# Performance work log

Measured on AMD Instinct MI355X. Metric: run time of the kernel, lower is better.

Reference implementation:

```python
import jax, jax.numpy as jnp
import numpy as np
import math

EMBED_DIM = 1024
NUM_HEADS = 16
HEAD_DIM = EMBED_DIM // NUM_HEADS
WINDOW_SIZE = 32  # one-sided; full window = 2*w+1 = 65
SCALING = math.sqrt(HEAD_DIM)


def setup_inputs() -> dict:
    key = jax.random.key(0)
    ks = jax.random.split(key, 9)
    B, S, E = 2, 2048, EMBED_DIM
    s = 1.0 / math.sqrt(E)
    inp = {
        "hidden_states": jax.random.normal(ks[0], (B, S, E), dtype=jnp.float32),
        "q_w": jax.random.uniform(ks[1], (E, E), jnp.float32, -s, s),
        "q_b": jax.random.uniform(ks[2], (E,), jnp.float32, -s, s),
        "k_w": jax.random.uniform(ks[3], (E, E), jnp.float32, -s, s),
        "k_b": jax.random.uniform(ks[4], (E,), jnp.float32, -s, s),
        "v_w": jax.random.uniform(ks[5], (E, E), jnp.float32, -s, s),
        "v_b": jax.random.uniform(ks[6], (E,), jnp.float32, -s, s),
        "o_w": jax.random.uniform(ks[7], (E, E), jnp.float32, -s, s),
        "o_b": jax.random.uniform(ks[8], (E,), jnp.float32, -s, s),
    }
    return inp


def reference(hidden_states, q_w, q_b, k_w, k_b, v_w, v_b, o_w, o_b):
    B, S, E = hidden_states.shape
    H, D, w = NUM_HEADS, HEAD_DIM, WINDOW_SIZE
    W = 2 * w + 1

    q = hidden_states @ q_w.T + q_b
    k = hidden_states @ k_w.T + k_b
    v = hidden_states @ v_w.T + v_b

    # [B, H, S, D]
    q = q.reshape(B, S, H, D).transpose(0, 2, 1, 3)
    k = k.reshape(B, S, H, D).transpose(0, 2, 1, 3)
    v = v.reshape(B, S, H, D).transpose(0, 2, 1, 3)

    # zero-pad seq dim by w on each side (matches F.pad value=0); padded keys
    # contribute score 0 (NOT -inf) exactly like the original unfold scheme.
    k_pad = jnp.pad(k, ((0, 0), (0, 0), (w, w), (0, 0)))
    v_pad = jnp.pad(v, ((0, 0), (0, 0), (w, w), (0, 0)))

    # window gather indices: query i sees padded positions i..i+2w (orig i-w..i+w)
    idx = jnp.arange(S)[:, None] + jnp.arange(W)[None, :]  # [S, W]
    k_slice = k_pad[:, :, idx]  # [B, H, S, W, D]
    v_slice = v_pad[:, :, idx]  # [B, H, S, W, D]

    score = jnp.einsum('bhsd,bhswd->bhsw', q, k_slice) / SCALING
    p = jax.nn.softmax(score, axis=-1)
    attn = jnp.einsum('bhsw,bhswd->bhsd', p, v_slice)

    attn = attn.transpose(0, 2, 1, 3).reshape(B, S, E)
    return attn @ o_w.T + o_b
```

## Files before the change

kernel.cpp:

```cpp
#include <hip/hip_runtime.h>
#include <math.h>

typedef _Float16 h16;
typedef _Float16 h8 __attribute__((ext_vector_type(8)));
typedef float f32x4 __attribute__((ext_vector_type(4)));

__device__ inline void gl2lds16(const void* g, void* l) {
  __builtin_amdgcn_global_load_lds(
      (const __attribute__((address_space(1))) void*)g,
      (__attribute__((address_space(3))) void*)l, 16, 0, 0);
}

__device__ inline void barrier_raw() {
  asm volatile("" ::: "memory");
  __builtin_amdgcn_s_barrier();
  asm volatile("" ::: "memory");
}

#define VMCNT(N) asm volatile("s_waitcnt vmcnt(" #N ")" ::: "memory")

__global__ __launch_bounds__(256) void f2h_all(
    const float* __restrict__ hs, const float* __restrict__ w0,
    const float* __restrict__ w1, const float* __restrict__ w2,
    const float* __restrict__ w3, h16* __restrict__ dst, int hsN) {
  int i = (blockIdx.x * 256 + threadIdx.x) * 8;
  const int tot = hsN + 4 * 1048576;
  if (i >= tot) return;
  const float* src;
  int off;
  if (i < hsN) {
    src = hs; off = i;
  } else {
    int k = i - hsN;
    int seg = k >> 20;
    off = k & 1048575;
    src = seg == 0 ? w0 : seg == 1 ? w1 : seg == 2 ? w2 : w3;
  }
  float4 a = *(const float4*)(src + off);
  float4 b = *(const float4*)(src + off + 4);
  h8 o;
  o[0] = (h16)a.x; o[1] = (h16)a.y; o[2] = (h16)a.z; o[3] = (h16)a.w;
  o[4] = (h16)b.x; o[5] = (h16)b.y; o[6] = (h16)b.z; o[7] = (h16)b.w;
  *(h8*)(dst + i) = o;
}

__global__ __launch_bounds__(256, 4) void qkv9(
    const h16* __restrict__ A, const h16* __restrict__ Bw,
    const float* __restrict__ qb, const float* __restrict__ kb,
    const float* __restrict__ vb, h16* __restrict__ qo, h16* __restrict__ ko,
    h16* __restrict__ vo) {
  __shared__ __align__(16) char smem[128 * 136 * 2];
  h16* Abuf = (h16*)smem;
  h16* Bbuf = Abuf + 2 * 128 * 32;
  h16* Csh = (h16*)smem;

  const int tid = threadIdx.x;
  const int wid = tid >> 6, lane = tid & 63;
  const int lr = lane & 15, lg = lane >> 4;
  const int wr = wid >> 1, wc = wid & 1;
  const int srow = tid >> 2;
  const int csw = ((tid & 3) ^ ((srow >> 1) & 3)) * 8;

  const int wg = (blockIdx.x & 7) * 96 + (blockIdx.x >> 3);
  const int bm = wg & 31, bn = wg >> 5;
  const int row0 = bm * 128, col0 = bn * 128;

  const h16* Ag = A + (size_t)row0 * 1024;
  const h16* Bg = Bw + (size_t)col0 * 1024;

  auto stage = [&](int t, int bi) {
    const int kof = t * 32 + csw;
    h16* Ad = Abuf + bi * 128 * 32;
    h16* Bd = Bbuf + bi * 128 * 32;
    gl2lds16(Ag + (size_t)srow * 1024 + kof, Ad + (wid * 16) * 32);
    gl2lds16(Ag + (size_t)(64 + srow) * 1024 + kof, Ad + (64 + wid * 16) * 32);
    gl2lds16(Bg + (size_t)srow * 1024 + kof, Bd + (wid * 16) * 32);
    gl2lds16(Bg + (size_t)(64 + srow) * 1024 + kof, Bd + (64 + wid * 16) * 32);
  };
  auto ldf = [&](const h16* base, int row) -> h8 {
    return *(const h8*)(base + row * 32 + (lg ^ ((row >> 1) & 3)) * 8);
  };

  f32x4 acc[4][4] = {};

  stage(0, 0);
  for (int t = 0; t < 32; ++t) {
    if (t < 31) {
      stage(t + 1, (t + 1) & 1);
      VMCNT(4);
    } else {
      VMCNT(0);
    }
    barrier_raw();
    const h16* Ar = Abuf + (t & 1) * 128 * 32;
    const h16* Br = Bbuf + (t & 1) * 128 * 32;
    h8 af[4], bf[4];
#pragma unroll
    for (int m = 0; m < 4; ++m) af[m] = ldf(Ar, wr * 64 + m * 16 + lr);
#pragma unroll
    for (int n = 0; n < 4; ++n) bf[n] = ldf(Br, wc * 64 + n * 16 + lr);
    __builtin_amdgcn_s_setprio(1);
#pragma unroll
    for (int m = 0; m < 4; ++m)
#pragma unroll
      for (int n = 0; n < 4; ++n)
        acc[m][n] =
            __builtin_amdgcn_mfma_f32_16x16x32_f16(af[m], bf[n], acc[m][n], 0, 0, 0);
    __builtin_amdgcn_s_setprio(0);
    barrier_raw();
  }

  const int tsel = bn >> 3;
  const int colseg = (bn & 7) * 128;
  const float* bp = tsel == 0 ? qb : (tsel == 1 ? kb : vb);
  h16* outp = tsel == 0 ? qo : (tsel == 1 ? ko : vo);

#pragma unroll
  for (int n = 0; n < 4; ++n) {
    const int ccol = wc * 64 + n * 16 + lr;
    const float bv = bp[colseg + ccol];
#pragma unroll
    for (int m = 0; m < 4; ++m)
#pragma unroll
      for (int j = 0; j < 4; ++j)
        Csh[(wr * 64 + m * 16 + lg * 4 + j) * 136 + ccol] =
            (h16)(acc[m][n][j] + bv);
  }
  barrier_raw();
#pragma unroll
  for (int p = 0; p < 8; ++p) {
    const int idx = p * 256 + tid;
    const int r = idx >> 4, c = idx & 15;
    h8 v = *(const h8*)&Csh[r * 136 + c * 8];
    *(h8*)&outp[(size_t)(row0 + r) * 1024 + colseg + c * 8] = v;
  }
}

__global__ __launch_bounds__(256) void oproj9(const h16* __restrict__ A,
                                              const h16* __restrict__ Bw,
                                              const float* __restrict__ b0,
                                              float* __restrict__ Cf) {
  __shared__ __align__(16) h16 Abuf[2][64][32];
  __shared__ __align__(16) h16 Bbuf[2][128][32];

  const int tid = threadIdx.x;
  const int wid = tid >> 6, lane = tid & 63;
  const int lr = lane & 15, lg = lane >> 4;
  const int wr = wid >> 1, wc = wid & 1;
  const int srow = tid >> 2;
  const int csw = ((tid & 3) ^ ((srow >> 1) & 3)) * 8;

  const int wg = (blockIdx.x & 7) * 64 + (blockIdx.x >> 3);
  const int bm = wg & 63, bn = wg >> 6;
  const int row0 = bm * 64, col0 = bn * 128;

  const h16* Ag = A + (size_t)row0 * 1024;
  const h16* Bg = Bw + (size_t)col0 * 1024;

  auto stage = [&](int t, int bi) {
    const int kof = t * 32 + csw;
    gl2lds16(Ag + (size_t)srow * 1024 + kof, &Abuf[bi][wid * 16][0]);
    gl2lds16(Bg + (size_t)srow * 1024 + kof, &Bbuf[bi][wid * 16][0]);
    gl2lds16(Bg + (size_t)(64 + srow) * 1024 + kof, &Bbuf[bi][64 + wid * 16][0]);
  };
  auto ldf = [&](const h16* base, int row) -> h8 {
    return *(const h8*)(base + row * 32 + (lg ^ ((row >> 1) & 3)) * 8);
  };

  f32x4 acc[2][4] = {};

  stage(0, 0);
  for (int t = 0; t < 32; ++t) {
    if (t < 31) {
      stage(t + 1, (t + 1) & 1);
      VMCNT(3);
    } else {
      VMCNT(0);
    }
    barrier_raw();
    const h16* Ar = &Abuf[t & 1][0][0];
    const h16* Br = &Bbuf[t & 1][0][0];
    h8 af[2], bf[4];
#pragma unroll
    for (int m = 0; m < 2; ++m) af[m] = ldf(Ar, wr * 32 + m * 16 + lr);
#pragma unroll
    for (int n = 0; n < 4; ++n) bf[n] = ldf(Br, wc * 64 + n * 16 + lr);
    __builtin_amdgcn_s_setprio(1);
#pragma unroll
    for (int m = 0; m < 2; ++m)
#pragma unroll
      for (int n = 0; n < 4; ++n)
        acc[m][n] =
            __builtin_amdgcn_mfma_f32_16x16x32_f16(af[m], bf[n], acc[m][n], 0, 0, 0);
    __builtin_amdgcn_s_setprio(0);
    barrier_raw();
  }

#pragma unroll
  for (int n = 0; n < 4; ++n) {
    const int cidx = col0 + wc * 64 + n * 16 + lr;
    const float bv = b0[cidx];
#pragma unroll
    for (int m = 0; m < 2; ++m)
#pragma unroll
      for (int j = 0; j < 4; ++j) {
        const int r = row0 + wr * 32 + m * 16 + lg * 4 + j;
        Cf[(size_t)r * 1024 + cidx] = acc[m][n][j] + bv;
      }
  }
}

__global__ __launch_bounds__(256) void swattn(const h16* __restrict__ Q,
                                              const h16* __restrict__ K,
                                              const h16* __restrict__ V,
                                              h16* __restrict__ O) {
  __shared__ __align__(16) h16 Ksh[128 * 72];
  __shared__ __align__(16) h16 Vsh[64 * 136];
  __shared__ __align__(16) h16 Psh[4][16 * 136];

  const int qb0 = blockIdx.x * 64;
  const int bh = blockIdx.y;
  const int b = bh >> 4, h = bh & 15;
  const int tid = threadIdx.x;
  const int wave = tid >> 6, lane = tid & 63;
  const int lr = lane & 15, lg = lane >> 4;

  const h16* Qb = Q + (size_t)b * 2048 * 1024 + h * 64;
  const h16* Kb = K + (size_t)b * 2048 * 1024 + h * 64;
  const h16* Vb = V + (size_t)b * 2048 * 1024 + h * 64;

#pragma unroll
  for (int i = 0; i < 4; ++i) {
    const int c = tid * 4 + i;
    const int row = c >> 3, c8 = c & 7;
    const int t = qb0 - 32 + row;
    h8 kv, vv;
    if (t >= 0 && t < 2048) {
      kv = *(const h8*)&Kb[(size_t)t * 1024 + c8 * 8];
      vv = *(const h8*)&Vb[(size_t)t * 1024 + c8 * 8];
    } else {
#pragma unroll
      for (int j = 0; j < 8; ++j) { kv[j] = (h16)0.f; vv[j] = (h16)0.f; }
    }
    *(h8*)&Ksh[row * 72 + c8 * 8] = kv;
#pragma unroll
    for (int j = 0; j < 8; ++j) Vsh[(c8 * 8 + j) * 136 + row] = vv[j];
  }
  __syncthreads();

  const int qrow = qb0 + wave * 16 + lr;
  h8 qa[2];
#pragma unroll
  for (int kk = 0; kk < 2; ++kk)
    qa[kk] = *(const h8*)&Qb[(size_t)qrow * 1024 + kk * 32 + lg * 8];

  f32x4 sacc[8] = {};
#pragma unroll
  for (int n = 0; n < 8; ++n)
#pragma unroll
    for (int kk = 0; kk < 2; ++kk) {
      h8 kb = *(const h8*)&Ksh[(n * 16 + lr) * 72 + kk * 32 + lg * 8];
      sacc[n] = __builtin_amdgcn_mfma_f32_16x16x32_f16(qa[kk], kb, sacc[n], 0, 0, 0);
    }

  float p[8][4];
#pragma unroll
  for (int j = 0; j < 4; ++j) {
    const int wrow = wave * 16 + lg * 4 + j;
    float mx = -1e30f;
#pragma unroll
    for (int n = 0; n < 8; ++n) {
      const int d = n * 16 + lr - wrow;
      float s = (d < 0 || d > 64) ? -1e30f : sacc[n][j] * 0.125f;
      p[n][j] = s;
      mx = fmaxf(mx, s);
    }
#pragma unroll
    for (int off = 1; off < 16; off <<= 1) mx = fmaxf(mx, __shfl_xor(mx, off, 64));
    float sum = 0.f;
#pragma unroll
    for (int n = 0; n < 8; ++n) {
      const float e = __expf(p[n][j] - mx);
      p[n][j] = e;
      sum += e;
    }
#pragma unroll
    for (int off = 1; off < 16; off <<= 1) sum += __shfl_xor(sum, off, 64);
    const float inv = 1.f / sum;
#pragma unroll
    for (int n = 0; n < 8; ++n) p[n][j] *= inv;
  }

#pragma unroll
  for (int n = 0; n < 8; ++n)
#pragma unroll
    for (int j = 0; j < 4; ++j)
      Psh[wave][(lg * 4 + j) * 136 + n * 16 + lr] = (h16)p[n][j];
  __syncthreads();

  f32x4 oacc[4] = {};
#pragma unroll
  for (int kk = 0; kk < 4; ++kk) {
    h8 pa = *(const h8*)&Psh[wave][lr * 136 + kk * 32 + lg * 8];
#pragma unroll
    for (int n = 0; n < 4; ++n) {
      h8 vb = *(const h8*)&Vsh[(n * 16 + lr) * 136 + kk * 32 + lg * 8];
      oacc[n] = __builtin_amdgcn_mfma_f32_16x16x32_f16(pa, vb, oacc[n], 0, 0, 0);
    }
  }

#pragma unroll
  for (int n = 0; n < 4; ++n)
#pragma unroll
    for (int j = 0; j < 4; ++j) {
      const int s = qb0 + wave * 16 + lg * 4 + j;
      const int d = n * 16 + lr;
      O[((size_t)b * 2048 + s) * 1024 + h * 64 + d] = (h16)oacc[n][j];
    }
}

extern "C" void kernel_launch(void* const* d_in, const int* in_sizes, int n_in,
                              void* d_out, int out_size, void* d_ws, size_t ws_size,
                              hipStream_t stream) {
  const float* hs = (const float*)d_in[0];
  const float* qw = (const float*)d_in[1];
  const float* qb = (const float*)d_in[2];
  const float* kw = (const float*)d_in[3];
  const float* kb = (const float*)d_in[4];
  const float* vw = (const float*)d_in[5];
  const float* vb = (const float*)d_in[6];
  const float* ow = (const float*)d_in[7];
  const float* ob = (const float*)d_in[8];

  const int M = in_sizes[0] / 1024;

  h16* hsH = (h16*)d_ws;
  h16* wqkv = hsH + (size_t)M * 1024;
  h16* woH = wqkv + (size_t)3072 * 1024;
  h16* qH = woH + (size_t)1024 * 1024;
  h16* kH = qH + (size_t)M * 1024;
  h16* vH = kH + (size_t)M * 1024;
  h16* attnH = vH + (size_t)M * 1024;

  const int tot = M * 1024 + 4 * 1048576;
  f2h_all<<<(tot / 8 + 255) / 256, 256, 0, stream>>>(hs, qw, kw, vw, ow, hsH,
                                                     M * 1024);

  qkv9<<<768, 256, 0, stream>>>(hsH, wqkv, qb, kb, vb, qH, kH, vH);

  swattn<<<dim3(32, M / 2048 * 16), 256, 0, stream>>>(qH, kH, vH, attnH);

  oproj9<<<512, 256, 0, stream>>>(attnH, woH, ob, (float*)d_out);
}
```

Measured before the change: 92.59 us.

## Remap GEMM tiles per XCD for L2 locality, single-buffer QKV staging

Both GEMMs change how block indices map to output tiles so each XCD works on a compact 8x12 (QKV) or 8-row-by-8-column (oproj) patch, aiming for more A/B tile reuse in each XCD's L2. The QKV kernel also drops double-buffered async LDS staging in favour of a single buffer with __syncthreads, and gives the epilogue its own shared-memory array. The occupancy hint of 4 blocks per CU is removed. This frees LDS and lowers register pressure, but it loses the overlap between global loads and MFMA work, so load latency is now exposed on every k-step.

New measurement: 86.89 us. 1.07x faster.

```diff
diff --git a/kernel.cpp b/kernel.cpp
--- a/kernel.cpp
+++ b/kernel.cpp
@@ -44,15 +44,14 @@
   *(h8*)(dst + i) = o;
 }
 
-__global__ __launch_bounds__(256, 4) void qkv9(
+__global__ __launch_bounds__(256) void qkv97(
     const h16* __restrict__ A, const h16* __restrict__ Bw,
     const float* __restrict__ qb, const float* __restrict__ kb,
     const float* __restrict__ vb, h16* __restrict__ qo, h16* __restrict__ ko,
     h16* __restrict__ vo) {
-  __shared__ __align__(16) char smem[128 * 136 * 2];
-  h16* Abuf = (h16*)smem;
-  h16* Bbuf = Abuf + 2 * 128 * 32;
-  h16* Csh = (h16*)smem;
+  __shared__ __align__(16) h16 Ash[128 * 32];
+  __shared__ __align__(16) h16 Bsh[128 * 32];
+  __shared__ __align__(16) h16 Csh[128 * 136];
 
   const int tid = threadIdx.x;
   const int wid = tid >> 6, lane = tid & 63;
@@ -61,44 +60,34 @@
   const int srow = tid >> 2;
   const int csw = ((tid & 3) ^ ((srow >> 1) & 3)) * 8;
 
-  const int wg = (blockIdx.x & 7) * 96 + (blockIdx.x >> 3);
-  const int bm = wg & 31, bn = wg >> 5;
+  const int xcd = blockIdx.x & 7;
+  const int i = blockIdx.x >> 3;
+  const int ibm = i & 7, ibn = i >> 3;
+  const int bm = (xcd & 3) * 8 + ibm;
+  const int bn = (xcd >> 2) * 12 + ibn;
   const int row0 = bm * 128, col0 = bn * 128;
 
   const h16* Ag = A + (size_t)row0 * 1024;
   const h16* Bg = Bw + (size_t)col0 * 1024;
 
-  auto stage = [&](int t, int bi) {
-    const int kof = t * 32 + csw;
-    h16* Ad = Abuf + bi * 128 * 32;
-    h16* Bd = Bbuf + bi * 128 * 32;
-    gl2lds16(Ag + (size_t)srow * 1024 + kof, Ad + (wid * 16) * 32);
-    gl2lds16(Ag + (size_t)(64 + srow) * 1024 + kof, Ad + (64 + wid * 16) * 32);
-    gl2lds16(Bg + (size_t)srow * 1024 + kof, Bd + (wid * 16) * 32);
-    gl2lds16(Bg + (size_t)(64 + srow) * 1024 + kof, Bd + (64 + wid * 16) * 32);
-  };
   auto ldf = [&](const h16* base, int row) -> h8 {
     return *(const h8*)(base + row * 32 + (lg ^ ((row >> 1) & 3)) * 8);
   };
 
   f32x4 acc[4][4] = {};
 
-  stage(0, 0);
   for (int t = 0; t < 32; ++t) {
-    if (t < 31) {
-      stage(t + 1, (t + 1) & 1);
-      VMCNT(4);
-    } else {
-      VMCNT(0);
-    }
-    barrier_raw();
-    const h16* Ar = Abuf + (t & 1) * 128 * 32;
-    const h16* Br = Bbuf + (t & 1) * 128 * 32;
+    const int kof = t * 32 + csw;
+    gl2lds16(Ag + (size_t)srow * 1024 + kof, &Ash[(wid * 16) * 32]);
+    gl2lds16(Ag + (size_t)(64 + srow) * 1024 + kof, &Ash[(64 + wid * 16) * 32]);
+    gl2lds16(Bg + (size_t)srow * 1024 + kof, &Bsh[(wid * 16) * 32]);
+    gl2lds16(Bg + (size_t)(64 + srow) * 1024 + kof, &Bsh[(64 + wid * 16) * 32]);
+    __syncthreads();
     h8 af[4], bf[4];
 #pragma unroll
-    for (int m = 0; m < 4; ++m) af[m] = ldf(Ar, wr * 64 + m * 16 + lr);
-#pragma unroll
-    for (int n = 0; n < 4; ++n) bf[n] = ldf(Br, wc * 64 + n * 16 + lr);
+    for (int m = 0; m < 4; ++m) af[m] = ldf(Ash, wr * 64 + m * 16 + lr);
+#pragma unroll
+    for (int n = 0; n < 4; ++n) bf[n] = ldf(Bsh, wc * 64 + n * 16 + lr);
     __builtin_amdgcn_s_setprio(1);
 #pragma unroll
     for (int m = 0; m < 4; ++m)
@@ -107,7 +96,7 @@
         acc[m][n] =
             __builtin_amdgcn_mfma_f32_16x16x32_f16(af[m], bf[n], acc[m][n], 0, 0, 0);
     __builtin_amdgcn_s_setprio(0);
-    barrier_raw();
+    __syncthreads();
   }
 
   const int tsel = bn >> 3;
@@ -126,7 +115,7 @@
         Csh[(wr * 64 + m * 16 + lg * 4 + j) * 136 + ccol] =
             (h16)(acc[m][n][j] + bv);
   }
-  barrier_raw();
+  __syncthreads();
 #pragma unroll
   for (int p = 0; p < 8; ++p) {
     const int idx = p * 256 + tid;
@@ -150,8 +139,10 @@
   const int srow = tid >> 2;
   const int csw = ((tid & 3) ^ ((srow >> 1) & 3)) * 8;
 
-  const int wg = (blockIdx.x & 7) * 64 + (blockIdx.x >> 3);
-  const int bm = wg & 63, bn = wg >> 6;
+  const int xcd = blockIdx.x & 7;
+  const int i = blockIdx.x >> 3;
+  const int bm = xcd * 8 + (i & 7);
+  const int bn = i >> 3;
   const int row0 = bm * 64, col0 = bn * 128;
 
   const h16* Ag = A + (size_t)row0 * 1024;
@@ -346,7 +337,7 @@
   f2h_all<<<(tot / 8 + 255) / 256, 256, 0, stream>>>(hs, qw, kw, vw, ow, hsH,
                                                      M * 1024);
 
-  qkv9<<<768, 256, 0, stream>>>(hsH, wqkv, qb, kb, vb, qH, kH, vH);
+  qkv97<<<768, 256, 0, stream>>>(hsH, wqkv, qb, kb, vb, qH, kH, vH);
 
   swattn<<<dim3(32, M / 2048 * 16), 256, 0, stream>>>(qH, kH, vH, attnH);
 
```
